# Optimization experiments

Measured on AMD Instinct MI355X. Metric: run time of the kernel, lower is better.

The kernel has to match this reference:

```python
import jax, jax.numpy as jnp
import numpy as np

B, S, IN, OUT, GS = 4, 2048, 4096, 16384, 32
G = IN // GS  # 128 groups per row


def setup_inputs() -> dict:
    key = jax.random.key(0)
    kx, ks, ki = jax.random.split(key, 3)
    x = jax.random.normal(kx, (B, S, IN), dtype=jnp.float32)
    # n_bits=2 initial codebook from the module
    codebook = jnp.array([-1.0, -0.25, 0.25, 1.0], dtype=jnp.float32)
    # scale is the log of per-group max-abs (use_exp_for_scale=True)
    scale = jax.random.normal(ks, (OUT, G, 1), dtype=jnp.float32) * 0.1 - 2.0
    indexes = jax.random.randint(ki, (OUT, G, GS), 0, 4, dtype=jnp.int32)
    return {"x": x, "codebook": codebook, "scale": scale, "indexes": indexes}


def reference(x, codebook, scale, indexes):
    # dequantize_weight: normalize codebook, gather per-element, exp-scale per group
    cb_norm = codebook / jnp.clip(jnp.max(jnp.abs(codebook)), 1e-8, None)
    w = cb_norm[indexes] * jnp.exp(scale)          # (OUT, G, GS)
    w = w.reshape(OUT, IN)                         # (OUT, IN)
    # F.linear(x, w) = x @ w.T
    return jnp.einsum("bsi,oi->bso", x, w)
```

## Files before the change

### kernel.cpp

```cpp
#include <hip/hip_runtime.h>
#include <stdint.h>


typedef unsigned short u16;
typedef __attribute__((ext_vector_type(8))) __bf16 bf16x8;
typedef __attribute__((ext_vector_type(4))) float f32x4;

__device__ __forceinline__ uint32_t f2bf(float f) {
  uint32_t u = __builtin_bit_cast(uint32_t, f);
  return (u + 0x7FFFu + ((u >> 16) & 1u)) >> 16;
}

__device__ __forceinline__ void gload16(const u16* g, u16* l) {
  __builtin_amdgcn_global_load_lds(
      (__attribute__((address_space(1))) void*)(g),
      (__attribute__((address_space(3))) void*)(l), 16, 0, 0);
}

__device__ __forceinline__ uint32_t sel4(uint32_t b0, uint32_t b1, uint32_t b2,
                                         uint32_t b3, int q) {
  uint32_t lo = (q & 1) ? b1 : b0;
  uint32_t hi = (q & 1) ? b3 : b2;
  return (q & 2) ? hi : lo;
}

__global__ __launch_bounds__(256) void cvt_x(const float* __restrict__ x,
                                             u16* __restrict__ xb, int n8) {
  int t = blockIdx.x * 256 + threadIdx.x;
  if (t >= n8) return;
  const float4* xp = reinterpret_cast<const float4*>(x) + (size_t)t * 2;
  float4 v0 = xp[0], v1 = xp[1];
  uint4 o;
  o.x = f2bf(v0.x) | (f2bf(v0.y) << 16);
  o.y = f2bf(v0.z) | (f2bf(v0.w) << 16);
  o.z = f2bf(v1.x) | (f2bf(v1.y) << 16);
  o.w = f2bf(v1.z) | (f2bf(v1.w) << 16);
  reinterpret_cast<uint4*>(xb)[t] = o;
}

__global__ __launch_bounds__(256) void dequant_w(
    const float* __restrict__ cb, const float* __restrict__ scale,
    const int* __restrict__ idx, u16* __restrict__ w, int ngroups) {
  int t = blockIdx.x * 256 + threadIdx.x;
  if (t >= ngroups) return;
  float m = fmaxf(fmaxf(fabsf(cb[0]), fabsf(cb[1])),
                  fmaxf(fabsf(cb[2]), fabsf(cb[3])));
  m = fmaxf(m, 1e-8f);
  float s = expf(scale[t]) / m;
  uint32_t b0 = f2bf(cb[0] * s), b1 = f2bf(cb[1] * s);
  uint32_t b2 = f2bf(cb[2] * s), b3 = f2bf(cb[3] * s);
  const int4* ip = reinterpret_cast<const int4*>(idx) + (size_t)t * 8;
  uint4* op = reinterpret_cast<uint4*>(w) + (size_t)t * 4;
#pragma unroll
  for (int v = 0; v < 4; ++v) {
    int4 qa = ip[v * 2], qb = ip[v * 2 + 1];
    uint4 o;
    o.x = sel4(b0, b1, b2, b3, qa.x) | (sel4(b0, b1, b2, b3, qa.y) << 16);
    o.y = sel4(b0, b1, b2, b3, qa.z) | (sel4(b0, b1, b2, b3, qa.w) << 16);
    o.z = sel4(b0, b1, b2, b3, qb.x) | (sel4(b0, b1, b2, b3, qb.y) << 16);
    o.w = sel4(b0, b1, b2, b3, qb.z) | (sel4(b0, b1, b2, b3, qb.w) << 16);
    op[v] = o;
  }
}

#define BM 256
#define BN 256
#define BK 64

__device__ __forceinline__ void memfence() { asm volatile("" ::: "memory"); }
__device__ __forceinline__ void BARx() {
  memfence();
  __builtin_amdgcn_s_barrier();
  memfence();
}

__global__ void __launch_bounds__(512, 2) gemm256(
    const u16* __restrict__ A, const u16* __restrict__ Bt,
    float* __restrict__ C, int M, int N, int K) {
  __shared__ u16 sm[2][2][BM * BK];

  const int nwg = gridDim.x;
  const int cpx = nwg >> 3;
  const int bid = blockIdx.x;
  const int swz = (bid & 7) * cpx + (bid >> 3);
  const int ntn = N / BN;
  const int m0 = (swz / ntn) * BM;
  const int n0 = (swz % ntn) * BN;

  const int tid = threadIdx.x;
  const int lane = tid & 63;
  const int wid = tid >> 6;
  const int wr = wid >> 2;
  const int wc = wid & 3;

  const int srow = wid * 8 + (lane >> 3);
  const int scol = (((lane & 7) ^ ((lane >> 3) & 7)) << 3);
  const u16* gA = A + (size_t)(m0 + srow) * K + scol;
  const u16* gB = Bt + (size_t)(n0 + srow) * K + scol;

#define STAGE(b, op, h, gp, kc)                                   \
  {                                                               \
    u16* d = &sm[(b)][(op)][(h)*8192 + wid * 512];                \
    const u16* g = (gp) + (size_t)((h)*128) * K + (kc);           \
    gload16(g, d);                                                \
    gload16(g + (size_t)64 * K, d + 4096);                        \
  }

  const int swzp0 = (((lane >> 4) ^ (lane & 7)) << 3);
  const int swzp1 = ((((lane >> 4) + 4) ^ (lane & 7)) << 3);
  const int lr = lane & 15;
  const int rAbase = (wr * 64 + lr) * BK;
  const int rBbase = (wc * 32 + lr) * BK;

  bf16x8 af[4][2], bv0[2][2], bv1[2][2];

#define LOADA(b, q)                                               \
  {                                                               \
    const u16* p = &sm[(b)][0][rAbase + (q)*8192];                \
    af[0][0] = *(const bf16x8*)(p + swzp0);                       \
    af[0][1] = *(const bf16x8*)(p + swzp1);                       \
    af[1][0] = *(const bf16x8*)(p + 1024 + swzp0);                \
    af[1][1] = *(const bf16x8*)(p + 1024 + swzp1);                \
    af[2][0] = *(const bf16x8*)(p + 2048 + swzp0);                \
    af[2][1] = *(const bf16x8*)(p + 2048 + swzp1);                \
    af[3][0] = *(const bf16x8*)(p + 3072 + swzp0);                \
    af[3][1] = *(const bf16x8*)(p + 3072 + swzp1);                \
  }
#define LOADBX(BV, b, pp)                                         \
  {                                                               \
    const u16* p = &sm[(b)][1][rBbase + (pp)*8192];               \
    BV[0][0] = *(const bf16x8*)(p + swzp0);                       \
    BV[0][1] = *(const bf16x8*)(p + swzp1);                       \
    BV[1][0] = *(const bf16x8*)(p + 1024 + swzp0);                \
    BV[1][1] = *(const bf16x8*)(p + 1024 + swzp1);                \
  }
#define MFMAQ(q, pp, BV)                                                    \
  {                                                                         \
    __builtin_amdgcn_s_setprio(1);                                          \
    _Pragma("unroll") for (int i = 0; i < 4; ++i)                           \
        _Pragma("unroll") for (int j = 0; j < 2; ++j)                       \
            _Pragma("unroll") for (int ks = 0; ks < 2; ++ks)                \
                acc[(q)*4 + i][(pp)*2 + j] =                                \
        __builtin_amdgcn_mfma_f32_16x16x32_bf16(                            \
            af[i][ks], BV[j][ks], acc[(q)*4 + i][(pp)*2 + j], 0, 0, 0);     \
    __builtin_amdgcn_s_setprio(0);                                          \
  }
#define VM6 asm volatile("s_waitcnt vmcnt(6)" ::: "memory");
#define VM0 asm volatile("s_waitcnt vmcnt(0)" ::: "memory");

  f32x4 acc[8][4];
#pragma unroll
  for (int i = 0; i < 8; ++i)
#pragma unroll
    for (int j = 0; j < 4; ++j) acc[i][j] = f32x4{0.f, 0.f, 0.f, 0.f};

  STAGE(0, 0, 0, gA, (size_t)0)
  STAGE(0, 1, 0, gB, (size_t)0)
  STAGE(0, 1, 1, gB, (size_t)0)
  STAGE(0, 0, 1, gA, (size_t)0)
  STAGE(1, 0, 0, gA, (size_t)64)
  STAGE(1, 1, 0, gB, (size_t)64)
  STAGE(1, 1, 1, gB, (size_t)64)
  VM6
  BARx();

#pragma unroll 1
  for (int i = 0; i < 31; ++i) {
    const size_t cT1 = (size_t)(2 * i + 1) * 64;
    const size_t cT2 = (size_t)(2 * i + 2) * 64;
    const size_t cT3 = (size_t)(2 * i + 3) * 64;
    LOADA(0, 0) LOADBX(bv0, 0, 0)
    STAGE(1, 0, 1, gA, cT1)
    BARx(); MFMAQ(0, 0, bv0)
    LOADBX(bv1, 0, 1)
    BARx(); MFMAQ(0, 1, bv1)
    LOADA(0, 1)
    STAGE(0, 0, 0, gA, cT2) STAGE(0, 1, 0, gB, cT2)
    BARx(); MFMAQ(1, 1, bv1)
    STAGE(0, 1, 1, gB, cT2)
    VM6
    BARx(); MFMAQ(1, 0, bv0)
    LOADA(1, 0) LOADBX(bv0, 1, 0)
    STAGE(0, 0, 1, gA, cT2)
    BARx(); MFMAQ(0, 0, bv0)
    LOADBX(bv1, 1, 1)
    BARx(); MFMAQ(0, 1, bv1)
    LOADA(1, 1)
    STAGE(1, 0, 0, gA, cT3) STAGE(1, 1, 0, gB, cT3)
    BARx(); MFMAQ(1, 1, bv1)
    STAGE(1, 1, 1, gB, cT3)
    VM6
    BARx(); MFMAQ(1, 0, bv0)
  }

  {
    const size_t cT1 = (size_t)63 * 64;
    LOADA(0, 0) LOADBX(bv0, 0, 0)
    STAGE(1, 0, 1, gA, cT1)
    BARx(); MFMAQ(0, 0, bv0)
    LOADBX(bv1, 0, 1)
    BARx(); MFMAQ(0, 1, bv1)
    LOADA(0, 1)
    BARx(); MFMAQ(1, 1, bv1)
    VM0
    BARx(); MFMAQ(1, 0, bv0)
    LOADA(1, 0) LOADBX(bv0, 1, 0)
    BARx(); MFMAQ(0, 0, bv0)
    LOADBX(bv1, 1, 1)
    BARx(); MFMAQ(0, 1, bv1)
    LOADA(1, 1)
    BARx(); MFMAQ(1, 1, bv1)
    BARx(); MFMAQ(1, 0, bv0)
  }

  const int crow0 = m0 + wr * 64 + ((lane >> 4) << 2);
  const int ccol0 = n0 + wc * 32 + (lane & 15);
#pragma unroll
  for (int q = 0; q < 2; ++q)
#pragma unroll
    for (int mi = 0; mi < 4; ++mi)
#pragma unroll
      for (int r = 0; r < 4; ++r) {
        float* cp = C + (size_t)(crow0 + q * 128 + mi * 16 + r) * N + ccol0;
#pragma unroll
        for (int pp = 0; pp < 2; ++pp)
#pragma unroll
          for (int j = 0; j < 2; ++j)
            cp[pp * 128 + j * 16] = acc[q * 4 + mi][pp * 2 + j][r];
      }
}

extern "C" void kernel_launch(void* const* d_in, const int* in_sizes, int n_in,
                              void* d_out, int out_size, void* d_ws,
                              size_t ws_size, hipStream_t stream) {
  const float* x = (const float*)d_in[0];
  const float* cb = (const float*)d_in[1];
  const float* scale = (const float*)d_in[2];
  const int* idx = (const int*)d_in[3];
  float* out = (float*)d_out;

  constexpr int M = 4 * 2048;
  constexpr int N = 16384;
  constexpr int K = 4096;

  u16* xb = (u16*)d_ws;
  u16* wb = xb + (size_t)M * K;

  const int n8 = M * K / 8;
  cvt_x<<<dim3(n8 / 256), dim3(256), 0, stream>>>(x, xb, n8);
  const int ngroups = N * (K / 32);
  dequant_w<<<dim3(ngroups / 256), dim3(256), 0, stream>>>(cb, scale, idx, wb,
                                                           ngroups);
  gemm256<<<dim3((M / BM) * (N / BN)), dim3(512), 0, stream>>>(xb, wb, out, M,
                                                               N, K);
}
```

Measured before the change: 1.027 ms.

## Double-buffer register fragments to prefetch LDS reads one MFMA phase ahead

Adds a second A fragment set and a third B fragment set so that LDS reads for the next MFMA block are issued before the current block's MFMAs instead of just before their own use. The first fragments move ahead of the loop, and the vmcnt waits are made finer-grained and spread across the phases. The goal is to hide LDS read latency behind MFMA work. The cost is a large rise in VGPR use, which may lower occupancy or cause spills, and the reordered waits and barriers add a risk of races on the shared-memory buffers.

```diff
diff --git a/kernel.cpp b/kernel.cpp
--- a/kernel.cpp
+++ b/kernel.cpp
@@ -112,19 +112,19 @@
   const int rAbase = (wr * 64 + lr) * BK;
   const int rBbase = (wc * 32 + lr) * BK;
 
-  bf16x8 af[4][2], bv0[2][2], bv1[2][2];
-
-#define LOADA(b, q)                                               \
+  bf16x8 afE[4][2], afO[4][2], bvA[2][2], bvB[2][2], bvC[2][2];
+
+#define LOADAX(AF, b, q)                                          \
   {                                                               \
     const u16* p = &sm[(b)][0][rAbase + (q)*8192];                \
-    af[0][0] = *(const bf16x8*)(p + swzp0);                       \
-    af[0][1] = *(const bf16x8*)(p + swzp1);                       \
-    af[1][0] = *(const bf16x8*)(p + 1024 + swzp0);                \
-    af[1][1] = *(const bf16x8*)(p + 1024 + swzp1);                \
-    af[2][0] = *(const bf16x8*)(p + 2048 + swzp0);                \
-    af[2][1] = *(const bf16x8*)(p + 2048 + swzp1);                \
-    af[3][0] = *(const bf16x8*)(p + 3072 + swzp0);                \
-    af[3][1] = *(const bf16x8*)(p + 3072 + swzp1);                \
+    AF[0][0] = *(const bf16x8*)(p + swzp0);                       \
+    AF[0][1] = *(const bf16x8*)(p + swzp1);                       \
+    AF[1][0] = *(const bf16x8*)(p + 1024 + swzp0);                \
+    AF[1][1] = *(const bf16x8*)(p + 1024 + swzp1);                \
+    AF[2][0] = *(const bf16x8*)(p + 2048 + swzp0);                \
+    AF[2][1] = *(const bf16x8*)(p + 2048 + swzp1);                \
+    AF[3][0] = *(const bf16x8*)(p + 3072 + swzp0);                \
+    AF[3][1] = *(const bf16x8*)(p + 3072 + swzp1);                \
   }
 #define LOADBX(BV, b, pp)                                         \
   {                                                               \
@@ -134,7 +134,7 @@
     BV[1][0] = *(const bf16x8*)(p + 1024 + swzp0);                \
     BV[1][1] = *(const bf16x8*)(p + 1024 + swzp1);                \
   }
-#define MFMAQ(q, pp, BV)                                                    \
+#define MFMAQ(q, pp, AF, BV)                                                \
   {                                                                         \
     __builtin_amdgcn_s_setprio(1);                                          \
     _Pragma("unroll") for (int i = 0; i < 4; ++i)                           \
@@ -142,11 +142,10 @@
             _Pragma("unroll") for (int ks = 0; ks < 2; ++ks)                \
                 acc[(q)*4 + i][(pp)*2 + j] =                                \
         __builtin_amdgcn_mfma_f32_16x16x32_bf16(                            \
-            af[i][ks], BV[j][ks], acc[(q)*4 + i][(pp)*2 + j], 0, 0, 0);     \
+            AF[i][ks], BV[j][ks], acc[(q)*4 + i][(pp)*2 + j], 0, 0, 0);     \
     __builtin_amdgcn_s_setprio(0);                                          \
   }
-#define VM6 asm volatile("s_waitcnt vmcnt(6)" ::: "memory");
-#define VM0 asm volatile("s_waitcnt vmcnt(0)" ::: "memory");
+#define VMW(n) asm volatile("s_waitcnt vmcnt(" #n ")" ::: "memory");
 
   f32x4 acc[8][4];
 #pragma unroll
@@ -161,56 +160,70 @@
   STAGE(1, 0, 0, gA, (size_t)64)
   STAGE(1, 1, 0, gB, (size_t)64)
   STAGE(1, 1, 1, gB, (size_t)64)
-  VM6
+  VMW(6)
   BARx();
+  LOADAX(afE, 0, 0)
+  LOADBX(bvA, 0, 0)
 
 #pragma unroll 1
   for (int i = 0; i < 31; ++i) {
     const size_t cT1 = (size_t)(2 * i + 1) * 64;
     const size_t cT2 = (size_t)(2 * i + 2) * 64;
     const size_t cT3 = (size_t)(2 * i + 3) * 64;
-    LOADA(0, 0) LOADBX(bv0, 0, 0)
     STAGE(1, 0, 1, gA, cT1)
-    BARx(); MFMAQ(0, 0, bv0)
-    LOADBX(bv1, 0, 1)
-    BARx(); MFMAQ(0, 1, bv1)
-    LOADA(0, 1)
-    STAGE(0, 0, 0, gA, cT2) STAGE(0, 1, 0, gB, cT2)
-    BARx(); MFMAQ(1, 1, bv1)
+    LOADBX(bvB, 0, 1)
+    VMW(8)
+    BARx(); MFMAQ(0, 0, afE, bvA)
+    LOADAX(afO, 0, 1)
+    STAGE(0, 0, 0, gA, cT2)
+    BARx(); MFMAQ(0, 1, afE, bvB)
+    STAGE(0, 1, 0, gB, cT2)
+    VMW(8)
+    BARx(); MFMAQ(1, 1, afO, bvB)
+    LOADAX(afE, 1, 0)
+    LOADBX(bvC, 1, 0)
     STAGE(0, 1, 1, gB, cT2)
-    VM6
-    BARx(); MFMAQ(1, 0, bv0)
-    LOADA(1, 0) LOADBX(bv0, 1, 0)
+    VMW(8)
+    BARx(); MFMAQ(1, 0, afO, bvA)
+    LOADBX(bvB, 1, 1)
     STAGE(0, 0, 1, gA, cT2)
-    BARx(); MFMAQ(0, 0, bv0)
-    LOADBX(bv1, 1, 1)
-    BARx(); MFMAQ(0, 1, bv1)
-    LOADA(1, 1)
-    STAGE(1, 0, 0, gA, cT3) STAGE(1, 1, 0, gB, cT3)
-    BARx(); MFMAQ(1, 1, bv1)
+    VMW(8)
+    BARx(); MFMAQ(0, 0, afE, bvC)
+    LOADAX(afO, 1, 1)
+    VMW(6)
+    BARx(); MFMAQ(0, 1, afE, bvB)
+    LOADAX(afE, 0, 0)
+    STAGE(1, 0, 0, gA, cT3)
+    STAGE(1, 1, 0, gB, cT3)
+    VMW(8)
+    BARx(); MFMAQ(1, 1, afO, bvB)
+    LOADBX(bvA, 0, 0)
     STAGE(1, 1, 1, gB, cT3)
-    VM6
-    BARx(); MFMAQ(1, 0, bv0)
+    VMW(8)
+    BARx(); MFMAQ(1, 0, afO, bvC)
   }
 
   {
     const size_t cT1 = (size_t)63 * 64;
-    LOADA(0, 0) LOADBX(bv0, 0, 0)
     STAGE(1, 0, 1, gA, cT1)
-    BARx(); MFMAQ(0, 0, bv0)
-    LOADBX(bv1, 0, 1)
-    BARx(); MFMAQ(0, 1, bv1)
-    LOADA(0, 1)
-    BARx(); MFMAQ(1, 1, bv1)
-    VM0
-    BARx(); MFMAQ(1, 0, bv0)
-    LOADA(1, 0) LOADBX(bv0, 1, 0)
-    BARx(); MFMAQ(0, 0, bv0)
-    LOADBX(bv1, 1, 1)
-    BARx(); MFMAQ(0, 1, bv1)
-    LOADA(1, 1)
-    BARx(); MFMAQ(1, 1, bv1)
-    BARx(); MFMAQ(1, 0, bv0)
+    LOADBX(bvB, 0, 1)
+    VMW(8)
+    BARx(); MFMAQ(0, 0, afE, bvA)
+    LOADAX(afO, 0, 1)
+    BARx(); MFMAQ(0, 1, afE, bvB)
+    VMW(4)
+    BARx(); MFMAQ(1, 1, afO, bvB)
+    LOADAX(afE, 1, 0)
+    LOADBX(bvC, 1, 0)
+    VMW(2)
+    BARx(); MFMAQ(1, 0, afO, bvA)
+    LOADBX(bvB, 1, 1)
+    VMW(0)
+    BARx(); MFMAQ(0, 0, afE, bvC)
+    LOADAX(afO, 1, 1)
+    BARx(); MFMAQ(0, 1, afE, bvB)
+    BARx(); MFMAQ(1, 1, afO, bvB)
+    BARx(); MFMAQ(1, 0, afO, bvC)
   }
 
   const int crow0 = m0 + wr * 64 + ((lane >> 4) << 2);
```

Measured after the change: 2.783 ms. 171% more time.
